# Kernel tuning notes

Measured on AMD Instinct MI355X. Metric: run time of the kernel, lower is better.

Reference implementation:

```python
import jax, jax.numpy as jnp
import numpy as np

DIM = 192
HEADS = 6
HSP = 8
WSP = 8
POS_DIM = (DIM // 4) // 4  # 12


def _ln(x, g, b, eps=1e-5):
    m = jnp.mean(x, -1, keepdims=True)
    v = jnp.mean((x - m) ** 2, -1, keepdims=True)
    return (x - m) / jnp.sqrt(v + eps) * g + b


def _rel_tables():
    # rpe_biases: ((2*HSP-1)*(2*WSP-1), 2) float coords of all relative offsets
    bh, bw = np.meshgrid(np.arange(1 - HSP, HSP), np.arange(1 - WSP, WSP), indexing='ij')
    biases = np.stack([bh, bw], -1).reshape(-1, 2).astype(np.float32)
    # relative_position_index: (N, N) int lookup into the bias table
    ch, cw = np.meshgrid(np.arange(HSP), np.arange(WSP), indexing='ij')
    coords = np.stack([ch, cw], 0).reshape(2, -1)  # (2, N)
    rel = coords[:, :, None] - coords[:, None, :]  # (2, N, N)
    idx = (rel[0] + HSP - 1) * (2 * WSP - 1) + (rel[1] + WSP - 1)
    return jnp.asarray(biases), jnp.asarray(idx.astype(np.int32))


def setup_inputs() -> dict:
    key = jax.random.key(0)
    ks = jax.random.split(key, 8)
    B, H, W = 2, 256, 256
    L = H * W
    def lin(k, i, o):
        return jax.random.normal(k, (i, o), jnp.float32) * 0.02
    return {
        'qkv': jax.random.normal(ks[0], (3, B, L, DIM), jnp.float32),
        'w_proj': lin(ks[1], 2, POS_DIM), 'b_proj': jnp.zeros((POS_DIM,), jnp.float32),
        'g1': jnp.ones((POS_DIM,), jnp.float32), 'be1': jnp.zeros((POS_DIM,), jnp.float32),
        'w1': lin(ks[2], POS_DIM, POS_DIM), 'b1': jnp.zeros((POS_DIM,), jnp.float32),
        'g2': jnp.ones((POS_DIM,), jnp.float32), 'be2': jnp.zeros((POS_DIM,), jnp.float32),
        'w2': lin(ks[3], POS_DIM, POS_DIM), 'b2': jnp.zeros((POS_DIM,), jnp.float32),
        'g3': jnp.ones((POS_DIM,), jnp.float32), 'be3': jnp.zeros((POS_DIM,), jnp.float32),
        'w3': lin(ks[4], POS_DIM, HEADS), 'b3': jnp.zeros((HEADS,), jnp.float32),
        'H': H, 'W': W,
    }


def reference(qkv, w_proj, b_proj, g1, be1, w1, b1, g2, be2, w2, b2, g3, be3, w3, b3, H, W):
    B, L, C = qkv.shape[1], qkv.shape[2], qkv.shape[3]
    hd = C // HEADS
    scale = float(hd) ** -0.5
    N = HSP * WSP

    def im2win(x):
        # (B, L, C) -> (B*nW, heads, N, hd)
        x = x.reshape(B, H // HSP, HSP, W // WSP, WSP, C)
        x = x.transpose(0, 1, 3, 2, 4, 5).reshape(-1, N, HEADS, hd)
        return x.transpose(0, 2, 1, 3)

    q = im2win(qkv[0]) * scale
    k = im2win(qkv[1])
    v = im2win(qkv[2])

    attn = jnp.einsum('whnd,whmd->whnm', q, k)  # (B*nW, heads, N, N)

    # dynamic relative position bias via MLP (DynamicPosBias, residual=False)
    biases, rel_idx = _rel_tables()
    p = biases @ w_proj + b_proj
    p = jax.nn.relu(_ln(p, g1, be1)) @ w1 + b1
    p = jax.nn.relu(_ln(p, g2, be2)) @ w2 + b2
    p = jax.nn.relu(_ln(p, g3, be3)) @ w3 + b3  # (n_rel, heads)
    rpb = p[rel_idx.reshape(-1)].reshape(N, N, HEADS).transpose(2, 0, 1)  # (heads, N, N)
    attn = attn + rpb[None]

    attn = jax.nn.softmax(attn, axis=-1)
    x = jnp.einsum('whnm,whmd->whnd', attn, v)  # (B*nW, heads, N, hd)
    x = x.transpose(0, 2, 1, 3).reshape(-1, N, C)

    # windows2img: (B*nW, N, C) -> (B, H, W, C)
    x = x.reshape(B, H // HSP, W // WSP, HSP, WSP, C)
    x = x.transpose(0, 1, 3, 2, 4, 5).reshape(B, H, W, C)
    return x
```

## Files before the change

kernel.cpp:

```cpp
#include <hip/hip_runtime.h>
#include <hip/hip_bf16.h>

#define NHEADS 6
#define HD 32
#define CDIM 192
#define NTOK 64
#define NREL 225
#define PDIM 12
#define IMG 256
#define NWIN 2048
#define QSCALE 0.2550348686f
#define LOG2E 1.4426950408889634f

typedef __attribute__((ext_vector_type(8))) short v8s;
typedef __attribute__((ext_vector_type(4))) float v4f;

#define KS2 200
#define VTS 72
#define PTS 72

__device__ __forceinline__ unsigned pkbf(float x, float y) {
    __hip_bfloat162 h = __float22bfloat162_rn(make_float2(x, y));
    union { __hip_bfloat162 h; unsigned u; } c; c.h = h;
    return c.u;
}

__device__ __forceinline__ float ex2(float x) {
    float r; asm("v_exp_f32 %0, %1" : "=v"(r) : "v"(x)); return r;
}

__device__ __forceinline__ void ln_relu12(const float* x, const float* g,
                                          const float* be, float* y) {
    float m = 0.f;
#pragma unroll
    for (int i = 0; i < PDIM; ++i) m += x[i];
    m *= (1.f / PDIM);
    float v = 0.f;
#pragma unroll
    for (int i = 0; i < PDIM; ++i) { float d = x[i] - m; v += d * d; }
    v *= (1.f / PDIM);
    float inv = rsqrtf(v + 1e-5f);
#pragma unroll
    for (int i = 0; i < PDIM; ++i) {
        float t = (x[i] - m) * inv * g[i] + be[i];
        y[i] = t > 0.f ? t : 0.f;
    }
}

__global__ __launch_bounds__(512, 4) void win_attn_fused(
    const float* __restrict__ qkv,
    const float* __restrict__ wp, const float* __restrict__ bp,
    const float* __restrict__ g1, const float* __restrict__ be1,
    const float* __restrict__ w1, const float* __restrict__ b1,
    const float* __restrict__ g2, const float* __restrict__ be2,
    const float* __restrict__ w2, const float* __restrict__ b2,
    const float* __restrict__ g3, const float* __restrict__ be3,
    const float* __restrict__ w3, const float* __restrict__ b3,
    float* __restrict__ out)
{
    __shared__ __align__(16) unsigned short ks[NTOK * KS2];
    __shared__ __align__(16) unsigned short vt[CDIM * VTS];
    __shared__ __align__(16) unsigned short pt[2][NTOK * PTS];
    __shared__ __align__(16) float pshf[NREL * 8];

    const int t = threadIdx.x;
    const int win = blockIdx.x;
    const int b  = win >> 10;
    const int bh = (win >> 5) & 31;
    const int bw = win & 31;

    const int lane = t & 63;
    const int wave = t >> 6;
    const int rg   = wave & 3;
    const int hh   = wave >> 2;
    const int hbase = hh * 3;
    const int lw = lane & 15;
    const int lg = lane >> 4;
    const int rowbase = rg * 16;

    const size_t PL = (size_t)2 * IMG * IMG * CDIM;
    const float* qplane = qkv + (size_t)b * IMG * IMG * CDIM;
    const float* kplane = qplane + PL;
    const float* vplane = kplane + PL;

    auto pixoff = [&](int tok) -> size_t {
        return ((size_t)(bh * 8 + (tok >> 3)) * IMG + (bw * 8 + (tok & 7))) * CDIM;
    };

#pragma unroll
    for (int pass = 0; pass < 6; ++pass) {
        int fidx = t + pass * 512;
        int s   = fidx / 384;
        int rem = fidx - s * 384;
        int j1  = rem / 48;
        int f   = rem - j1 * 48;
        float4 k4 = *(const float4*)(kplane
                     + ((size_t)(bh * 8 + s) * IMG + (bw * 8 + j1)) * CDIM + f * 4);
        uint2 kk; kk.x = pkbf(k4.x, k4.y); kk.y = pkbf(k4.z, k4.w);
        *(uint2*)&ks[(s * 8 + j1) * KS2 + f * 4] = kk;
    }

    {
        const int u  = t & 31;
        const int dg = (t >> 5) & 7;
        const int vh = t >> 8;
        const int ta = (u & 15) + (u >> 4) * 32;
        const int db = dg * 4;
        const int kpa = (u & 15) * 4 + (u >> 4) * 2;
        const size_t offa = pixoff(ta), offb = pixoff(ta + 16);
#pragma unroll
        for (int hi = 0; hi < 3; ++hi) {
            int h = vh * 3 + hi;
            float4 va = *(const float4*)(vplane + offa + h * HD + db);
            float4 vb = *(const float4*)(vplane + offb + h * HD + db);
            int row = h * HD + db;
            *(unsigned*)&vt[(row + 0) * VTS + kpa] = pkbf(va.x, vb.x);
            *(unsigned*)&vt[(row + 1) * VTS + kpa] = pkbf(va.y, vb.y);
            *(unsigned*)&vt[(row + 2) * VTS + kpa] = pkbf(va.z, vb.z);
            *(unsigned*)&vt[(row + 3) * VTS + kpa] = pkbf(va.w, vb.w);
        }
    }

    v8s aq[3];
    {
        const size_t qoff = pixoff(rowbase + lw);
#pragma unroll
        for (int hi = 0; hi < 3; ++hi) {
            const float* qp = qplane + qoff + (hbase + hi) * HD + lg * 8;
            float4 q0 = *(const float4*)qp;
            float4 q1 = *(const float4*)(qp + 4);
            union { v8s v; unsigned x[4]; } au;
            au.x[0] = pkbf(q0.x * QSCALE, q0.y * QSCALE);
            au.x[1] = pkbf(q0.z * QSCALE, q0.w * QSCALE);
            au.x[2] = pkbf(q1.x * QSCALE, q1.y * QSCALE);
            au.x[3] = pkbf(q1.z * QSCALE, q1.w * QSCALE);
            aq[hi] = au.v;
        }
    }

    if (t < NREL) {
        float x0 = (float)(t / 15 - 7);
        float x1 = (float)(t % 15 - 7);
        float h[PDIM], y[PDIM];
#pragma unroll
        for (int o = 0; o < PDIM; ++o)
            h[o] = x0 * wp[o] + x1 * wp[PDIM + o] + bp[o];
        ln_relu12(h, g1, be1, y);
#pragma unroll
        for (int o = 0; o < PDIM; ++o) {
            float a = b1[o];
#pragma unroll
            for (int i = 0; i < PDIM; ++i) a += y[i] * w1[i * PDIM + o];
            h[o] = a;
        }
        ln_relu12(h, g2, be2, y);
#pragma unroll
        for (int o = 0; o < PDIM; ++o) {
            float a = b2[o];
#pragma unroll
            for (int i = 0; i < PDIM; ++i) a += y[i] * w2[i * PDIM + o];
            h[o] = a;
        }
        ln_relu12(h, g3, be3, y);
        const int sw = (t >> 2) & 1;
#pragma unroll
        for (int o = 0; o < NHEADS; ++o) {
            float a = b3[o];
#pragma unroll
            for (int i = 0; i < PDIM; ++i) a += y[i] * w3[i * NHEADS + o];
            int half = (o >= 3) ? 1 : 0;
            pshf[(t * 2 + (half ^ sw)) * 4 + (o - half * 3)] = a * LOG2E;
        }
    }
    __syncthreads();

    int base_r[4];
#pragma unroll
    for (int r = 0; r < 4; ++r) {
        int n = rowbase + lg * 4 + r;
        base_r[r] = ((n >> 3) - (lw >> 3) + 7) * 15 + (n & 7) - (lw & 7) + 7;
    }

    v4f acc[3][4];
#pragma unroll
    for (int ct = 0; ct < 4; ++ct) {
#pragma unroll
        for (int hi = 0; hi < 3; ++hi) {
            v4f z = {0.f, 0.f, 0.f, 0.f};
            v8s bfr = *(const v8s*)&ks[(ct * 16 + lw) * KS2 + (hbase + hi) * HD + lg * 8];
            acc[hi][ct] = __builtin_amdgcn_mfma_f32_16x16x32_bf16(aq[hi], bfr, z, 0, 0, 0);
        }
    }

#pragma unroll
    for (int ct = 0; ct < 4; ++ct)
#pragma unroll
        for (int r = 0; r < 4; ++r) {
            int idx = base_r[r] - ct * 30;
            const float4 bb = *(const float4*)&pshf[(idx * 2 + (hh ^ ((idx >> 2) & 1))) * 4];
            acc[0][ct][r] = ex2(acc[0][ct][r] + bb.x);
            acc[1][ct][r] = ex2(acc[1][ct][r] + bb.y);
            acc[2][ct][r] = ex2(acc[2][ct][r] + bb.z);
        }

    size_t ooff[4];
#pragma unroll
    for (int r = 0; r < 4; ++r) {
        int n = rowbase + lg * 4 + r;
        ooff[r] = ((size_t)(b * IMG + bh * 8 + (n >> 3)) * IMG
                   + (bw * 8 + (n & 7))) * CDIM;
    }

    v8s ones;
#pragma unroll
    for (int j = 0; j < 8; ++j) ones[j] = (short)0x3F80;

#pragma unroll
    for (int hi = 0; hi < 3; ++hi) {
        const int h = hbase + hi;
#pragma unroll
        for (int r = 0; r < 4; ++r) {
            uint2 w;
            w.x = pkbf(acc[hi][0][r], acc[hi][1][r]);
            w.y = pkbf(acc[hi][2][r], acc[hi][3][r]);
            *(uint2*)&pt[hh][(rowbase + lg * 4 + r) * PTS + lw * 4] = w;
        }
        v8s pa[2];
#pragma unroll
        for (int kt = 0; kt < 2; ++kt)
            pa[kt] = *(const v8s*)&pt[hh][(rowbase + lw) * PTS + kt * 32 + lg * 8];
        v4f acc2[2] = {};
        v4f acc3 = {0.f, 0.f, 0.f, 0.f};
#pragma unroll
        for (int kt = 0; kt < 2; ++kt) {
#pragma unroll
            for (int dt = 0; dt < 2; ++dt) {
                v8s vb = *(const v8s*)&vt[(h * HD + dt * 16 + lw) * VTS
                                          + kt * 32 + lg * 8];
                acc2[dt] = __builtin_amdgcn_mfma_f32_16x16x32_bf16(pa[kt], vb, acc2[dt], 0, 0, 0);
            }
            acc3 = __builtin_amdgcn_mfma_f32_16x16x32_bf16(pa[kt], ones, acc3, 0, 0, 0);
        }
        v4f rinv;
#pragma unroll
        for (int r = 0; r < 4; ++r) rinv[r] = __builtin_amdgcn_rcpf(acc3[r]);
#pragma unroll
        for (int dt = 0; dt < 2; ++dt)
#pragma unroll
            for (int r = 0; r < 4; ++r)
                out[ooff[r] + h * HD + dt * 16 + lw] = acc2[dt][r] * rinv[r];
    }
}

extern "C" void kernel_launch(void* const* d_in, const int* in_sizes, int n_in,
                              void* d_out, int out_size, void* d_ws, size_t ws_size,
                              hipStream_t stream) {
    const float* qkv = (const float*)d_in[0];
    win_attn_fused<<<NWIN, 512, 0, stream>>>(
        qkv,
        (const float*)d_in[1], (const float*)d_in[2],
        (const float*)d_in[3], (const float*)d_in[4],
        (const float*)d_in[5], (const float*)d_in[6],
        (const float*)d_in[7], (const float*)d_in[8],
        (const float*)d_in[9], (const float*)d_in[10],
        (const float*)d_in[11], (const float*)d_in[12],
        (const float*)d_in[13], (const float*)d_in[14],
        (float*)d_out);
}
```

Measured before the change: 88.82 us.

## Keep softmax probabilities in registers via transposed QK MFMA and permuted V layout

Swaps the MFMA operands for QK^T so each lane holds a query row's scores, which lets the probabilities feed the PV MFMA straight from registers. This removes the P round-trip through shared memory and the extra ones-MFMA used for row sums; normalization is now a cross-lane shuffle sum done before the bf16 pack. V is loaded as pairs of tokens into a permuted key order that matches the register layout, and K/V global loads are issued early with their LDS stores deferred, to overlap memory latency with the bias MLP. It adds a second barrier and keeps more registers live, which may hurt occupancy under the 512x4 launch bounds.

```diff
diff --git a/kernel.cpp b/kernel.cpp
--- a/kernel.cpp
+++ b/kernel.cpp
@@ -17,7 +17,6 @@
 
 #define KS2 200
 #define VTS 72
-#define PTS 72
 
 __device__ __forceinline__ unsigned pkbf(float x, float y) {
     __hip_bfloat162 h = __float22bfloat162_rn(make_float2(x, y));
@@ -60,7 +59,6 @@
 {
     __shared__ __align__(16) unsigned short ks[NTOK * KS2];
     __shared__ __align__(16) unsigned short vt[CDIM * VTS];
-    __shared__ __align__(16) unsigned short pt[2][NTOK * PTS];
     __shared__ __align__(16) float pshf[NREL * 8];
 
     const int t = threadIdx.x;
@@ -87,6 +85,8 @@
         return ((size_t)(bh * 8 + (tok >> 3)) * IMG + (bw * 8 + (tok & 7))) * CDIM;
     };
 
+    float4 kreg[6];
+    int kidx[6][2];
 #pragma unroll
     for (int pass = 0; pass < 6; ++pass) {
         int fidx = t + pass * 512;
@@ -94,30 +94,23 @@
         int rem = fidx - s * 384;
         int j1  = rem / 48;
         int f   = rem - j1 * 48;
-        float4 k4 = *(const float4*)(kplane
+        kreg[pass] = *(const float4*)(kplane
                      + ((size_t)(bh * 8 + s) * IMG + (bw * 8 + j1)) * CDIM + f * 4);
-        uint2 kk; kk.x = pkbf(k4.x, k4.y); kk.y = pkbf(k4.z, k4.w);
-        *(uint2*)&ks[(s * 8 + j1) * KS2 + f * 4] = kk;
-    }
-
-    {
-        const int u  = t & 31;
-        const int dg = (t >> 5) & 7;
-        const int vh = t >> 8;
-        const int ta = (u & 15) + (u >> 4) * 32;
-        const int db = dg * 4;
-        const int kpa = (u & 15) * 4 + (u >> 4) * 2;
-        const size_t offa = pixoff(ta), offb = pixoff(ta + 16);
-#pragma unroll
-        for (int hi = 0; hi < 3; ++hi) {
-            int h = vh * 3 + hi;
-            float4 va = *(const float4*)(vplane + offa + h * HD + db);
-            float4 vb = *(const float4*)(vplane + offb + h * HD + db);
-            int row = h * HD + db;
-            *(unsigned*)&vt[(row + 0) * VTS + kpa] = pkbf(va.x, vb.x);
-            *(unsigned*)&vt[(row + 1) * VTS + kpa] = pkbf(va.y, vb.y);
-            *(unsigned*)&vt[(row + 2) * VTS + kpa] = pkbf(va.z, vb.z);
-            *(unsigned*)&vt[(row + 3) * VTS + kpa] = pkbf(va.w, vb.w);
+        kidx[pass][0] = s * 8 + j1;
+        kidx[pass][1] = f * 4;
+    }
+
+    const int tp = t & 31;
+    const int g  = t >> 5;
+    const int tok0 = 2 * tp;
+    float4 vA[3], vB[3];
+    {
+        const size_t offa = pixoff(tok0), offb = pixoff(tok0 + 1);
+#pragma unroll
+        for (int i = 0; i < 3; ++i) {
+            int f = g + i * 16;
+            vA[i] = *(const float4*)(vplane + offa + f * 4);
+            vB[i] = *(const float4*)(vplane + offb + f * 4);
         }
     }
 
@@ -172,14 +165,15 @@
             pshf[(t * 2 + (half ^ sw)) * 4 + (o - half * 3)] = a * LOG2E;
         }
     }
+
+#pragma unroll
+    for (int pass = 0; pass < 6; ++pass) {
+        uint2 kk;
+        kk.x = pkbf(kreg[pass].x, kreg[pass].y);
+        kk.y = pkbf(kreg[pass].z, kreg[pass].w);
+        *(uint2*)&ks[kidx[pass][0] * KS2 + kidx[pass][1]] = kk;
+    }
     __syncthreads();
-
-    int base_r[4];
-#pragma unroll
-    for (int r = 0; r < 4; ++r) {
-        int n = rowbase + lg * 4 + r;
-        base_r[r] = ((n >> 3) - (lw >> 3) + 7) * 15 + (n & 7) - (lw & 7) + 7;
-    }
 
     v4f acc[3][4];
 #pragma unroll
@@ -188,20 +182,59 @@
         for (int hi = 0; hi < 3; ++hi) {
             v4f z = {0.f, 0.f, 0.f, 0.f};
             v8s bfr = *(const v8s*)&ks[(ct * 16 + lw) * KS2 + (hbase + hi) * HD + lg * 8];
-            acc[hi][ct] = __builtin_amdgcn_mfma_f32_16x16x32_bf16(aq[hi], bfr, z, 0, 0, 0);
-        }
-    }
-
-#pragma unroll
-    for (int ct = 0; ct < 4; ++ct)
-#pragma unroll
-        for (int r = 0; r < 4; ++r) {
-            int idx = base_r[r] - ct * 30;
-            const float4 bb = *(const float4*)&pshf[(idx * 2 + (hh ^ ((idx >> 2) & 1))) * 4];
-            acc[0][ct][r] = ex2(acc[0][ct][r] + bb.x);
-            acc[1][ct][r] = ex2(acc[1][ct][r] + bb.y);
-            acc[2][ct][r] = ex2(acc[2][ct][r] + bb.z);
-        }
+            acc[hi][ct] = __builtin_amdgcn_mfma_f32_16x16x32_bf16(bfr, aq[hi], z, 0, 0, 0);
+        }
+    }
+
+    {
+        const int q = rowbase + lw;
+        const int base2 = ((q >> 3) + 7) * 15 + (q & 7) + 7
+                        - ((lg >> 1) * 15 + (lg & 1) * 4);
+#pragma unroll
+        for (int ct = 0; ct < 4; ++ct)
+#pragma unroll
+            for (int r = 0; r < 4; ++r) {
+                int idx = base2 - ct * 30 - r;
+                const float4 bb = *(const float4*)&pshf[(idx * 2 + (hh ^ ((idx >> 2) & 1))) * 4];
+                acc[0][ct][r] = ex2(acc[0][ct][r] + bb.x);
+                acc[1][ct][r] = ex2(acc[1][ct][r] + bb.y);
+                acc[2][ct][r] = ex2(acc[2][ct][r] + bb.z);
+            }
+    }
+
+    unsigned pa[3][2][4];
+#pragma unroll
+    for (int hi = 0; hi < 3; ++hi) {
+        float s = 0.f;
+#pragma unroll
+        for (int ct = 0; ct < 4; ++ct)
+#pragma unroll
+            for (int r = 0; r < 4; ++r) s += acc[hi][ct][r];
+        s += __shfl_xor(s, 16);
+        s += __shfl_xor(s, 32);
+        float rv = __builtin_amdgcn_rcpf(s);
+#pragma unroll
+        for (int kt = 0; kt < 2; ++kt) {
+            pa[hi][kt][0] = pkbf(acc[hi][2*kt][0] * rv, acc[hi][2*kt][1] * rv);
+            pa[hi][kt][1] = pkbf(acc[hi][2*kt][2] * rv, acc[hi][2*kt][3] * rv);
+            pa[hi][kt][2] = pkbf(acc[hi][2*kt+1][0] * rv, acc[hi][2*kt+1][1] * rv);
+            pa[hi][kt][3] = pkbf(acc[hi][2*kt+1][2] * rv, acc[hi][2*kt+1][3] * rv);
+        }
+    }
+
+    {
+        const int k0 = ((tok0 >> 5) << 5) + (((tok0 >> 2) & 3) << 3)
+                     + (((tok0 >> 4) & 1) << 2) + (tok0 & 3);
+#pragma unroll
+        for (int i = 0; i < 3; ++i) {
+            int d0 = (g + i * 16) * 4;
+            *(unsigned*)&vt[(d0 + 0) * VTS + k0] = pkbf(vA[i].x, vB[i].x);
+            *(unsigned*)&vt[(d0 + 1) * VTS + k0] = pkbf(vA[i].y, vB[i].y);
+            *(unsigned*)&vt[(d0 + 2) * VTS + k0] = pkbf(vA[i].z, vB[i].z);
+            *(unsigned*)&vt[(d0 + 3) * VTS + k0] = pkbf(vA[i].w, vB[i].w);
+        }
+    }
+    __syncthreads();
 
     size_t ooff[4];
 #pragma unroll
@@ -211,44 +244,25 @@
                    + (bw * 8 + (n & 7))) * CDIM;
     }
 
-    v8s ones;
-#pragma unroll
-    for (int j = 0; j < 8; ++j) ones[j] = (short)0x3F80;
-
 #pragma unroll
     for (int hi = 0; hi < 3; ++hi) {
         const int h = hbase + hi;
-#pragma unroll
-        for (int r = 0; r < 4; ++r) {
-            uint2 w;
-            w.x = pkbf(acc[hi][0][r], acc[hi][1][r]);
-            w.y = pkbf(acc[hi][2][r], acc[hi][3][r]);
-            *(uint2*)&pt[hh][(rowbase + lg * 4 + r) * PTS + lw * 4] = w;
-        }
-        v8s pa[2];
-#pragma unroll
-        for (int kt = 0; kt < 2; ++kt)
-            pa[kt] = *(const v8s*)&pt[hh][(rowbase + lw) * PTS + kt * 32 + lg * 8];
         v4f acc2[2] = {};
-        v4f acc3 = {0.f, 0.f, 0.f, 0.f};
 #pragma unroll
         for (int kt = 0; kt < 2; ++kt) {
+            v8s pav = *(const v8s*)&pa[hi][kt][0];
 #pragma unroll
             for (int dt = 0; dt < 2; ++dt) {
                 v8s vb = *(const v8s*)&vt[(h * HD + dt * 16 + lw) * VTS
                                           + kt * 32 + lg * 8];
-                acc2[dt] = __builtin_amdgcn_mfma_f32_16x16x32_bf16(pa[kt], vb, acc2[dt], 0, 0, 0);
+                acc2[dt] = __builtin_amdgcn_mfma_f32_16x16x32_bf16(pav, vb, acc2[dt], 0, 0, 0);
             }
-            acc3 = __builtin_amdgcn_mfma_f32_16x16x32_bf16(pa[kt], ones, acc3, 0, 0, 0);
-        }
-        v4f rinv;
-#pragma unroll
-        for (int r = 0; r < 4; ++r) rinv[r] = __builtin_amdgcn_rcpf(acc3[r]);
+        }
 #pragma unroll
         for (int dt = 0; dt < 2; ++dt)
 #pragma unroll
             for (int r = 0; r < 4; ++r)
-                out[ooff[r] + h * HD + dt * 16 + lw] = acc2[dt][r] * rinv[r];
+                out[ooff[r] + h * HD + dt * 16 + lw] = acc2[dt][r];
     }
 }
 
```

After: 110.8 us. 24.8% more time.
